# Optimization experiments

Hardware: AMD Instinct MI355X
Metric: run time of the kernel (lower is better)

Reference implementation:

```python
import jax, jax.numpy as jnp
import numpy as np
from jax.ops import segment_sum, segment_max

N_NODES = 10000
N_EDGES = 160000
N_GRAPHS = 32
IN_DIM = 128
HID = 256
HEADS = 4


def setup_inputs() -> dict:
    key = jax.random.key(0)
    ks = jax.random.split(key, 12)
    x = jax.random.normal(ks[0], (N_NODES, IN_DIM), dtype=jnp.float32)
    edge_index = jax.random.randint(ks[1], (2, N_EDGES), 0, N_NODES, dtype=jnp.int64)
    batch = jnp.sort(jax.random.randint(ks[2], (N_NODES,), 0, N_GRAPHS, dtype=jnp.int64))
    s = 0.05
    params = {
        "W1": jax.random.normal(ks[3], (IN_DIM, HID), dtype=jnp.float32) * s,
        "b1": jnp.zeros((HID,), dtype=jnp.float32),
        "W2": jax.random.normal(ks[4], (HID, HID), dtype=jnp.float32) * s,
        "b2": jnp.zeros((HID,), dtype=jnp.float32),
        "Wg": jax.random.normal(ks[5], (HID, HEADS * HID), dtype=jnp.float32) * s,
        "att_src": jax.random.normal(ks[6], (HEADS, HID), dtype=jnp.float32) * s,
        "att_dst": jax.random.normal(ks[7], (HEADS, HID), dtype=jnp.float32) * s,
        "bg": jnp.zeros((HID,), dtype=jnp.float32),
        "W_heads": jax.random.normal(ks[8], (HID, 4), dtype=jnp.float32) * s,
        "b_heads": jnp.zeros((4,), dtype=jnp.float32),
    }
    return {"x": x, "edge_index": edge_index, "batch": batch, **params}


def _add_self_loops(edge_index, n):
    loop = jnp.arange(n, dtype=edge_index.dtype)
    src = jnp.concatenate([edge_index[0], loop])
    dst = jnp.concatenate([edge_index[1], loop])
    return src, dst


def _gcn_conv(x, W, b, src, dst, n):
    # PyG GCNConv: add self-loops, symmetric normalization D^-1/2 A D^-1/2
    h = x @ W                                   # [N, out]
    deg = segment_sum(jnp.ones_like(src, dtype=h.dtype), dst, num_segments=n)
    dinv = jax.lax.rsqrt(jnp.maximum(deg, 1e-12))
    coef = dinv[src] * dinv[dst]                # [E+N]
    out = segment_sum(h[src] * coef[:, None], dst, num_segments=n)
    return out + b


def _gat_conv(x, Wg, att_src, att_dst, bg, src, dst, n):
    # PyG GATConv(heads=4, concat=False): mean over heads, leaky_relu slope 0.2
    h = (x @ Wg).reshape(n, HEADS, HID)         # [N, H, C]
    a_src = jnp.einsum('nhc,hc->nh', h, att_src)
    a_dst = jnp.einsum('nhc,hc->nh', h, att_dst)
    e = jax.nn.leaky_relu(a_src[src] + a_dst[dst], 0.2)   # [E+N, H]
    m = segment_max(e, dst, num_segments=n)
    e = jnp.exp(e - m[dst])
    z = segment_sum(e, dst, num_segments=n)
    alpha = e / (z[dst] + 1e-16)                # softmax over edges into each dst
    out = segment_sum(h[src] * alpha[:, :, None], dst, num_segments=n)  # [N, H, C]
    return out.mean(axis=1) + bg


def reference(x, edge_index, batch, W1, b1, W2, b2, Wg, att_src, att_dst, bg, W_heads, b_heads):
    n = x.shape[0]
    src, dst = _add_self_loops(edge_index, n)
    h1 = jax.nn.relu(_gcn_conv(x, W1, b1, src, dst, n))
    h2 = jax.nn.relu(_gcn_conv(h1, W2, b2, src, dst, n))
    h3 = jax.nn.relu(_gat_conv(h2, Wg, att_src, att_dst, bg, src, dst, n))
    # global_mean_pool
    ones = jnp.ones((n,), dtype=h3.dtype)
    cnt = segment_sum(ones, batch, num_segments=N_GRAPHS)
    pooled = segment_sum(h3, batch, num_segments=N_GRAPHS) / jnp.maximum(cnt, 1.0)[:, None]
    # four scalar heads stacked: cols = [energy_absorption, elastic_modulus, ballistic_limit, penetration_resistance]
    return pooled @ W_heads + b_heads           # [G, 4]
```

## Files before the change

kernel.cpp:

```cpp
#include <hip/hip_runtime.h>
#include <cmath>

#define IN_DIM 128
#define HID 256
#define NHEADS 4
#define NGRAPHS 32

typedef unsigned short u16;
typedef __attribute__((ext_vector_type(8))) short bfrag8;
typedef __attribute__((ext_vector_type(4))) float f32x4;

__device__ __forceinline__ u16 f2bf(float x) {
  unsigned u = __float_as_uint(x);
  unsigned r = (u + 0x7fffu + ((u >> 16) & 1u)) >> 16;
  return (u16)r;
}
__device__ __forceinline__ float bf2f(u16 v) {
  return __uint_as_float(((unsigned)v) << 16);
}
__device__ __forceinline__ float lof(unsigned u) { return __uint_as_float(u << 16); }
__device__ __forceinline__ float hif(unsigned u) { return __uint_as_float(u & 0xffff0000u); }
__device__ __forceinline__ float lrelu02(float x) { return x > 0.f ? x : 0.2f * x; }

__global__ __launch_bounds__(256) void count_edges_k(const int* __restrict__ dst,
                                                     int* __restrict__ cnt, int E) {
  int i = blockIdx.x * 256 + threadIdx.x;
  if (i < E) atomicAdd(&cnt[dst[i]], 1);
}

__global__ __launch_bounds__(1024) void scan_k(const int* __restrict__ cnt,
                                               int* __restrict__ row_ptr,
                                               float* __restrict__ dinv, int n) {
  __shared__ int s_w[16];
  __shared__ int s_tot;
  int tid = threadIdx.x;
  int wv = tid >> 6, lane = tid & 63;
  int carry = 0;
  int nch = (n + 1023) >> 10;
  for (int c = 0; c < nch; c++) {
    int i = (c << 10) + tid;
    int v = (i < n) ? cnt[i] : 0;
    int incl = v;
    #pragma unroll
    for (int off = 1; off < 64; off <<= 1) {
      int t = __shfl_up(incl, off);
      if (lane >= off) incl += t;
    }
    if (lane == 63) s_w[wv] = incl;
    __syncthreads();
    if (tid < 16) {
      int sv = s_w[tid];
      int si = sv;
      #pragma unroll
      for (int off = 1; off < 16; off <<= 1) {
        int t = __shfl_up(si, off, 16);
        if (tid >= off) si += t;
      }
      s_w[tid] = si - sv;
      if (tid == 15) s_tot = si;
    }
    __syncthreads();
    int excl = incl - v + s_w[wv] + carry;
    if (i < n) {
      row_ptr[i] = excl;
      dinv[i] = rsqrtf((float)(v + 1));
    }
    carry += s_tot;
    __syncthreads();
  }
  if (tid == 0) row_ptr[n] = carry;
}

__global__ __launch_bounds__(256) void fill_csr_k(const int* __restrict__ src,
                                                  const int* __restrict__ dst,
                                                  const int* __restrict__ row_ptr,
                                                  int* __restrict__ cursor,
                                                  int* __restrict__ csr_src, int E) {
  int i = blockIdx.x * 256 + threadIdx.x;
  if (i < E) {
    int d = dst[i];
    int p = atomicAdd(&cursor[d], 1);
    csr_src[row_ptr[d] + p] = src[i];
  }
}

__device__ void pack_a_dev(const float* __restrict__ A, u16* __restrict__ Ap,
                           int K, int KT, int wid, int lane) {
  int fm = wid / KT, kt = wid - fm * KT;
  int m = fm * 16 + (lane & 15);
  int kb = kt * 32 + (lane >> 4) * 8;
  const float* src = A + (size_t)m * K + kb;
  float4 v0 = *(const float4*)src;
  float4 v1 = *(const float4*)(src + 4);
  float vv[8] = {v0.x, v0.y, v0.z, v0.w, v1.x, v1.y, v1.z, v1.w};
  u16 hi[8], lo[8];
  #pragma unroll
  for (int j = 0; j < 8; j++) {
    u16 h = f2bf(vv[j]);
    hi[j] = h;
    lo[j] = f2bf(vv[j] - bf2f(h));
  }
  u16* dstp = Ap + ((size_t)fm * KT + kt) * 1024 + lane * 8;
  *(ushort4*)(dstp)       = make_ushort4(hi[0], hi[1], hi[2], hi[3]);
  *(ushort4*)(dstp + 4)   = make_ushort4(hi[4], hi[5], hi[6], hi[7]);
  *(ushort4*)(dstp + 512) = make_ushort4(lo[0], lo[1], lo[2], lo[3]);
  *(ushort4*)(dstp + 516) = make_ushort4(lo[4], lo[5], lo[6], lo[7]);
}

__device__ void pack_b_dev(const float* __restrict__ B, u16* __restrict__ Bp,
                           int N, int KT, int wid, int lane) {
  int fn = wid / KT, kt = wid - fn * KT;
  int n = fn * 16 + (lane & 15);
  int kb = kt * 32 + (lane >> 4) * 8;
  float vv[8];
  #pragma unroll
  for (int j = 0; j < 8; j++) vv[j] = B[(size_t)(kb + j) * N + n];
  u16 hi[8], lo[8];
  #pragma unroll
  for (int j = 0; j < 8; j++) {
    u16 h = f2bf(vv[j]);
    hi[j] = h;
    lo[j] = f2bf(vv[j] - bf2f(h));
  }
  u16* dstp = Bp + ((size_t)fn * KT + kt) * 1024 + lane * 8;
  *(ushort4*)(dstp)       = make_ushort4(hi[0], hi[1], hi[2], hi[3]);
  *(ushort4*)(dstp + 4)   = make_ushort4(hi[4], hi[5], hi[6], hi[7]);
  *(ushort4*)(dstp + 512) = make_ushort4(lo[0], lo[1], lo[2], lo[3]);
  *(ushort4*)(dstp + 516) = make_ushort4(lo[4], lo[5], lo[6], lo[7]);
}

__global__ __launch_bounds__(256) void prep_k(const float* __restrict__ x,
                                              const float* __restrict__ W1,
                                              const float* __restrict__ W2,
                                              const float* __restrict__ Wg,
                                              const float* __restrict__ att_src,
                                              const float* __restrict__ att_dst,
                                              u16* __restrict__ xp,
                                              u16* __restrict__ w1p,
                                              u16* __restrict__ w2p,
                                              u16* __restrict__ wgp,
                                              float* __restrict__ w_s,
                                              float* __restrict__ w_d, int NFM) {
  __shared__ float red_s[4][NHEADS];
  __shared__ float red_d[4][NHEADS];
  int b = blockIdx.x;
  int tid = threadIdx.x;
  int lane = tid & 63;
  int XB = NFM;
  if (b < XB) {
    int wid = b * 4 + (tid >> 6);
    if (wid < NFM * 4) pack_a_dev(x, xp, IN_DIM, 4, wid, lane);
  } else if (b < XB + 16) {
    pack_b_dev(W1, w1p, HID, 4, (b - XB) * 4 + (tid >> 6), lane);
  } else if (b < XB + 48) {
    pack_b_dev(W2, w2p, HID, 8, (b - XB - 16) * 4 + (tid >> 6), lane);
  } else if (b < XB + 176) {
    pack_b_dev(Wg, wgp, NHEADS * HID, 8, (b - XB - 48) * 4 + (tid >> 6), lane);
  } else {
    int k = b - (XB + 176);
    int c = tid, wvv = c >> 6, ln = c & 63;
    #pragma unroll
    for (int h = 0; h < NHEADS; h++) {
      float w = Wg[(size_t)k * (NHEADS * HID) + h * HID + c];
      float vs = w * att_src[h * HID + c];
      float vd = w * att_dst[h * HID + c];
      #pragma unroll
      for (int off = 32; off; off >>= 1) {
        vs += __shfl_xor(vs, off);
        vd += __shfl_xor(vd, off);
      }
      if (ln == 0) { red_s[wvv][h] = vs; red_d[wvv][h] = vd; }
    }
    __syncthreads();
    if (c < NHEADS)
      w_s[k * NHEADS + c] = red_s[0][c] + red_s[1][c] + red_s[2][c] + red_s[3][c];
    else if (c < 2 * NHEADS) {
      int h = c - NHEADS;
      w_d[k * NHEADS + h] = red_d[0][h] + red_d[1][h] + red_d[2][h] + red_d[3][h];
    }
  }
}

template <int KT, int LDC, bool ALO>
__global__ __launch_bounds__(256) void mfma_gemm_k(const u16* __restrict__ Ap,
                                                   const u16* __restrict__ Bp,
                                                   u16* __restrict__ Cb, int M) {
  int tid = threadIdx.x;
  int w = tid >> 6, lane = tid & 63;
  int wm = w >> 1, wn = w & 1;
  int fm0 = blockIdx.y * 4 + wm * 2;
  int fn0 = blockIdx.x * 4 + wn * 2;
  f32x4 acc[2][2] = {};
  #pragma unroll
  for (int kt = 0; kt < KT; kt++) {
    bfrag8 a_hi[2], a_lo[2], b_hi[2], b_lo[2];
    #pragma unroll
    for (int f = 0; f < 2; f++) {
      const u16* pa = Ap + ((size_t)(fm0 + f) * KT + kt) * 1024 + lane * 8;
      a_hi[f] = *(const bfrag8*)pa;
      if constexpr (ALO) a_lo[f] = *(const bfrag8*)(pa + 512);
      const u16* pb = Bp + ((size_t)(fn0 + f) * KT + kt) * 1024 + lane * 8;
      b_hi[f] = *(const bfrag8*)pb;
      b_lo[f] = *(const bfrag8*)(pb + 512);
    }
    #pragma unroll
    for (int f = 0; f < 2; f++) {
      #pragma unroll
      for (int g = 0; g < 2; g++) {
        acc[f][g] = __builtin_amdgcn_mfma_f32_16x16x32_bf16(a_hi[f], b_hi[g], acc[f][g], 0, 0, 0);
        acc[f][g] = __builtin_amdgcn_mfma_f32_16x16x32_bf16(a_hi[f], b_lo[g], acc[f][g], 0, 0, 0);
        if constexpr (ALO)
          acc[f][g] = __builtin_amdgcn_mfma_f32_16x16x32_bf16(a_lo[f], b_hi[g], acc[f][g], 0, 0, 0);
      }
    }
  }
  int r0 = (lane >> 4) * 4;
  int cl = lane & 15;
  #pragma unroll
  for (int f = 0; f < 2; f++) {
    #pragma unroll
    for (int g = 0; g < 2; g++) {
      int col = (fn0 + g) * 16 + cl;
      #pragma unroll
      for (int r = 0; r < 4; r++) {
        int row = (fm0 + f) * 16 + r0 + r;
        if (row < M) Cb[(size_t)row * LDC + col] = f2bf(acc[f][g][r]);
      }
    }
  }
}

template <bool LOGITS, bool PACK_LO>
__global__ __launch_bounds__(256) void gcn_agg_k(const u16* __restrict__ t,
                                                 const int* __restrict__ row_ptr,
                                                 const int* __restrict__ csr_src,
                                                 const float* __restrict__ dinv,
                                                 const float* __restrict__ bias,
                                                 u16* __restrict__ apack,
                                                 const float* __restrict__ w_s,
                                                 const float* __restrict__ w_d,
                                                 float4* __restrict__ a_src4,
                                                 float4* __restrict__ a_dst4, int N) {
  int wv = threadIdx.x >> 6, lane = threadIdx.x & 63;
  int i = blockIdx.x * 4 + wv;
  if (i >= N) return;
  float di = dinv[i];
  int c4 = lane * 4;
  int beg = row_ptr[i], end = row_ptr[i + 1];
  float a0, a1, a2, a3;
  {
    uint2 u = *(const uint2*)&t[(size_t)i * HID + c4];
    float w = di * di;
    a0 = w * lof(u.x); a1 = w * hif(u.x); a2 = w * lof(u.y); a3 = w * hif(u.y);
  }
  int e = beg;
  for (; e + 3 < end; e += 4) {
    int s0 = csr_src[e + 0], s1 = csr_src[e + 1];
    int s2 = csr_src[e + 2], s3 = csr_src[e + 3];
    float w0 = dinv[s0] * di, w1 = dinv[s1] * di;
    float w2 = dinv[s2] * di, w3 = dinv[s3] * di;
    uint2 u0 = *(const uint2*)&t[(size_t)s0 * HID + c4];
    uint2 u1 = *(const uint2*)&t[(size_t)s1 * HID + c4];
    uint2 u2 = *(const uint2*)&t[(size_t)s2 * HID + c4];
    uint2 u3 = *(const uint2*)&t[(size_t)s3 * HID + c4];
    a0 += w0 * lof(u0.x) + w1 * lof(u1.x) + w2 * lof(u2.x) + w3 * lof(u3.x);
    a1 += w0 * hif(u0.x) + w1 * hif(u1.x) + w2 * hif(u2.x) + w3 * hif(u3.x);
    a2 += w0 * lof(u0.y) + w1 * lof(u1.y) + w2 * lof(u2.y) + w3 * lof(u3.y);
    a3 += w0 * hif(u0.y) + w1 * hif(u1.y) + w2 * hif(u2.y) + w3 * hif(u3.y);
  }
  for (; e < end; e++) {
    int s = csr_src[e];
    float w = dinv[s] * di;
    uint2 u = *(const uint2*)&t[(size_t)s * HID + c4];
    a0 += w * lof(u.x); a1 += w * hif(u.x); a2 += w * lof(u.y); a3 += w * hif(u.y);
  }
  float4 bv = *(const float4*)&bias[c4];
  float v0 = fmaxf(a0 + bv.x, 0.f), v1 = fmaxf(a1 + bv.y, 0.f);
  float v2 = fmaxf(a2 + bv.z, 0.f), v3 = fmaxf(a3 + bv.w, 0.f);
  {
    int fm = i >> 4, kt = c4 >> 5;
    int pl = (i & 15) + 16 * ((c4 >> 3) & 3);
    int j0 = c4 & 7;
    size_t base = ((size_t)fm * 8 + kt) * 1024 + pl * 8 + j0;
    u16 h0 = f2bf(v0), h1 = f2bf(v1), h2 = f2bf(v2), h3 = f2bf(v3);
    *(ushort4*)&apack[base] = make_ushort4(h0, h1, h2, h3);
    if constexpr (PACK_LO)
      *(ushort4*)&apack[base + 512] =
          make_ushort4(f2bf(v0 - bf2f(h0)), f2bf(v1 - bf2f(h1)),
                       f2bf(v2 - bf2f(h2)), f2bf(v3 - bf2f(h3)));
  }
  if constexpr (LOGITS) {
    const float4* ws4 = (const float4*)w_s;
    const float4* wd4 = (const float4*)w_d;
    float4 s0 = ws4[c4 + 0], s1 = ws4[c4 + 1], s2 = ws4[c4 + 2], s3 = ws4[c4 + 3];
    float4 d0 = wd4[c4 + 0], d1 = wd4[c4 + 1], d2 = wd4[c4 + 2], d3 = wd4[c4 + 3];
    float ps0 = v0 * s0.x + v1 * s1.x + v2 * s2.x + v3 * s3.x;
    float ps1 = v0 * s0.y + v1 * s1.y + v2 * s2.y + v3 * s3.y;
    float ps2 = v0 * s0.z + v1 * s1.z + v2 * s2.z + v3 * s3.z;
    float ps3 = v0 * s0.w + v1 * s1.w + v2 * s2.w + v3 * s3.w;
    float pd0 = v0 * d0.x + v1 * d1.x + v2 * d2.x + v3 * d3.x;
    float pd1 = v0 * d0.y + v1 * d1.y + v2 * d2.y + v3 * d3.y;
    float pd2 = v0 * d0.z + v1 * d1.z + v2 * d2.z + v3 * d3.z;
    float pd3 = v0 * d0.w + v1 * d1.w + v2 * d2.w + v3 * d3.w;
    #pragma unroll
    for (int off = 32; off; off >>= 1) {
      ps0 += __shfl_xor(ps0, off); ps1 += __shfl_xor(ps1, off);
      ps2 += __shfl_xor(ps2, off); ps3 += __shfl_xor(ps3, off);
      pd0 += __shfl_xor(pd0, off); pd1 += __shfl_xor(pd1, off);
      pd2 += __shfl_xor(pd2, off); pd3 += __shfl_xor(pd3, off);
    }
    if (lane == 0) {
      a_src4[i] = make_float4(ps0, ps1, ps2, ps3);
      a_dst4[i] = make_float4(pd0, pd1, pd2, pd3);
    }
  }
}

#define ACC8(U, AW, O)                                         \
  acc[O + 0] += (AW) * lof((U).x); acc[O + 1] += (AW) * hif((U).x); \
  acc[O + 2] += (AW) * lof((U).y); acc[O + 3] += (AW) * hif((U).y); \
  acc[O + 4] += (AW) * lof((U).z); acc[O + 5] += (AW) * hif((U).z); \
  acc[O + 6] += (AW) * lof((U).w); acc[O + 7] += (AW) * hif((U).w);

__global__ __launch_bounds__(256) void gat_agg_k(const u16* __restrict__ hgT,
                                                 const int* __restrict__ row_ptr,
                                                 const int* __restrict__ csr_src,
                                                 const float4* __restrict__ a_src4,
                                                 const float4* __restrict__ a_dst4,
                                                 const float* __restrict__ bg,
                                                 float* __restrict__ out, int N) {
  __shared__ int s_src[4][64];
  __shared__ float s_al[4][NHEADS][65];
  int wv = threadIdx.x >> 6, lane = threadIdx.x & 63;
  int i = blockIdx.x * 4 + wv;
  if (i >= N) return;
  int beg = row_ptr[i], end = row_ptr[i + 1];
  int deg = end - beg;
  float4 ad = a_dst4[i];
  int hw = lane >> 4;
  float acc[16];
  #pragma unroll
  for (int j = 0; j < 16; j++) acc[j] = 0.f;
  const u16* rowbase = hgT + (size_t)lane * 16;

  int nk;
  if (deg <= 63) {
    int s = (lane < deg) ? csr_src[beg + lane] : i;
    bool valid = (lane <= deg);
    float4 as = a_src4[s];
    float l0 = valid ? lrelu02(as.x + ad.x) : -INFINITY;
    float l1 = valid ? lrelu02(as.y + ad.y) : -INFINITY;
    float l2 = valid ? lrelu02(as.z + ad.z) : -INFINITY;
    float l3 = valid ? lrelu02(as.w + ad.w) : -INFINITY;
    float m0 = l0, m1 = l1, m2 = l2, m3 = l3;
    #pragma unroll
    for (int off = 32; off; off >>= 1) {
      m0 = fmaxf(m0, __shfl_xor(m0, off)); m1 = fmaxf(m1, __shfl_xor(m1, off));
      m2 = fmaxf(m2, __shfl_xor(m2, off)); m3 = fmaxf(m3, __shfl_xor(m3, off));
    }
    float e0 = valid ? expf(l0 - m0) : 0.f;
    float e1 = valid ? expf(l1 - m1) : 0.f;
    float e2 = valid ? expf(l2 - m2) : 0.f;
    float e3 = valid ? expf(l3 - m3) : 0.f;
    float z0 = e0, z1 = e1, z2 = e2, z3 = e3;
    #pragma unroll
    for (int off = 32; off; off >>= 1) {
      z0 += __shfl_xor(z0, off); z1 += __shfl_xor(z1, off);
      z2 += __shfl_xor(z2, off); z3 += __shfl_xor(z3, off);
    }
    s_src[wv][lane] = s;
    s_al[wv][0][lane] = e0 / (z0 + 1e-16f);
    s_al[wv][1][lane] = e1 / (z1 + 1e-16f);
    s_al[wv][2][lane] = e2 / (z2 + 1e-16f);
    s_al[wv][3][lane] = e3 / (z3 + 1e-16f);
    nk = deg + 1;
    int e = 0;
    for (; e + 1 < nk; e += 2) {
      int sa = s_src[wv][e], sb = s_src[wv][e + 1];
      float awa = s_al[wv][hw][e], awb = s_al[wv][hw][e + 1];
      const uint4* ra = (const uint4*)(rowbase + (size_t)sa * 1024);
      const uint4* rb = (const uint4*)(rowbase + (size_t)sb * 1024);
      uint4 ua0 = ra[0], ua1 = ra[1];
      uint4 ub0 = rb[0], ub1 = rb[1];
      ACC8(ua0, awa, 0); ACC8(ua1, awa, 8);
      ACC8(ub0, awb, 0); ACC8(ub1, awb, 8);
    }
    if (e < nk) {
      int sa = s_src[wv][e];
      float awa = s_al[wv][hw][e];
      const uint4* ra = (const uint4*)(rowbase + (size_t)sa * 1024);
      uint4 ua0 = ra[0], ua1 = ra[1];
      ACC8(ua0, awa, 0); ACC8(ua1, awa, 8);
    }
  } else {
    float4 asi = a_src4[i];
    float ls0 = lrelu02(asi.x + ad.x), ls1 = lrelu02(asi.y + ad.y);
    float ls2 = lrelu02(asi.z + ad.z), ls3 = lrelu02(asi.w + ad.w);
    float m0 = ls0, m1 = ls1, m2 = ls2, m3 = ls3;
    for (int e = beg + lane; e < end; e += 64) {
      float4 as = a_src4[csr_src[e]];
      m0 = fmaxf(m0, lrelu02(as.x + ad.x)); m1 = fmaxf(m1, lrelu02(as.y + ad.y));
      m2 = fmaxf(m2, lrelu02(as.z + ad.z)); m3 = fmaxf(m3, lrelu02(as.w + ad.w));
    }
    #pragma unroll
    for (int off = 32; off; off >>= 1) {
      m0 = fmaxf(m0, __shfl_xor(m0, off)); m1 = fmaxf(m1, __shfl_xor(m1, off));
      m2 = fmaxf(m2, __shfl_xor(m2, off)); m3 = fmaxf(m3, __shfl_xor(m3, off));
    }
    float z0 = (lane == 0) ? expf(ls0 - m0) : 0.f;
    float z1 = (lane == 0) ? expf(ls1 - m1) : 0.f;
    float z2 = (lane == 0) ? expf(ls2 - m2) : 0.f;
    float z3 = (lane == 0) ? expf(ls3 - m3) : 0.f;
    for (int e = beg + lane; e < end; e += 64) {
      float4 as = a_src4[csr_src[e]];
      z0 += expf(lrelu02(as.x + ad.x) - m0); z1 += expf(lrelu02(as.y + ad.y) - m1);
      z2 += expf(lrelu02(as.z + ad.z) - m2); z3 += expf(lrelu02(as.w + ad.w) - m3);
    }
    #pragma unroll
    for (int off = 32; off; off >>= 1) {
      z0 += __shfl_xor(z0, off); z1 += __shfl_xor(z1, off);
      z2 += __shfl_xor(z2, off); z3 += __shfl_xor(z3, off);
    }
    float iz0 = 1.f / (z0 + 1e-16f), iz1 = 1.f / (z1 + 1e-16f);
    float iz2 = 1.f / (z2 + 1e-16f), iz3 = 1.f / (z3 + 1e-16f);
    {
      float w0 = expf(ls0 - m0) * iz0, w1 = expf(ls1 - m1) * iz1;
      float w2 = expf(ls2 - m2) * iz2, w3 = expf(ls3 - m3) * iz3;
      float aw = hw == 0 ? w0 : hw == 1 ? w1 : hw == 2 ? w2 : w3;
      const uint4* r = (const uint4*)(rowbase + (size_t)i * 1024);
      uint4 u0 = r[0], u1 = r[1];
      ACC8(u0, aw, 0); ACC8(u1, aw, 8);
    }
    for (int base = beg; base < end; base += 64) {
      int mc = min(64, end - base);
      if (lane < mc) {
        int s = csr_src[base + lane];
        float4 as = a_src4[s];
        s_src[wv][lane] = s;
        s_al[wv][0][lane] = expf(lrelu02(as.x + ad.x) - m0) * iz0;
        s_al[wv][1][lane] = expf(lrelu02(as.y + ad.y) - m1) * iz1;
        s_al[wv][2][lane] = expf(lrelu02(as.z + ad.z) - m2) * iz2;
        s_al[wv][3][lane] = expf(lrelu02(as.w + ad.w) - m3) * iz3;
      }
      for (int e = 0; e < mc; e++) {
        int sa = s_src[wv][e];
        float awa = s_al[wv][hw][e];
        const uint4* ra = (const uint4*)(rowbase + (size_t)sa * 1024);
        uint4 ua0 = ra[0], ua1 = ra[1];
        ACC8(ua0, awa, 0); ACC8(ua1, awa, 8);
      }
    }
  }
  #pragma unroll
  for (int j = 0; j < 16; j++) {
    acc[j] += __shfl_xor(acc[j], 16);
    acc[j] += __shfl_xor(acc[j], 32);
  }
  if (lane < 16) {
    int cb = lane * 16;
    float o[16];
    #pragma unroll
    for (int j = 0; j < 16; j++)
      o[j] = fmaxf(acc[j] * 0.25f + bg[cb + j], 0.f);
    float* op = out + (size_t)i * HID + cb;
    *(float4*)(op + 0)  = make_float4(o[0], o[1], o[2], o[3]);
    *(float4*)(op + 4)  = make_float4(o[4], o[5], o[6], o[7]);
    *(float4*)(op + 8)  = make_float4(o[8], o[9], o[10], o[11]);
    *(float4*)(op + 12) = make_float4(o[12], o[13], o[14], o[15]);
  }
}

#define POOL_CHUNK 50
__global__ __launch_bounds__(256) void pool_acc_k(const float* __restrict__ h3,
                                                  const int* __restrict__ batch,
                                                  float* __restrict__ pooled,
                                                  float* __restrict__ gcnt, int N) {
  int c = threadIdx.x;
  int i0 = blockIdx.x * POOL_CHUNK;
  int i1 = min(i0 + POOL_CHUNK, N);
  if (i0 >= N) return;
  float acc = 0.f;
  int cur = batch[i0];
  int cnt_local = 0;
  for (int i = i0; i < i1; i++) {
    int g = batch[i];
    if (g != cur) {
      atomicAdd(&pooled[cur * HID + c], acc);
      if (c == 0) atomicAdd(&gcnt[cur], (float)cnt_local);
      acc = 0.f;
      cnt_local = 0;
      cur = g;
    }
    acc += h3[(size_t)i * HID + c];
    cnt_local++;
  }
  atomicAdd(&pooled[cur * HID + c], acc);
  if (c == 0) atomicAdd(&gcnt[cur], (float)cnt_local);
}

__global__ __launch_bounds__(128) void head_k(const float* __restrict__ pooled,
                                              const float* __restrict__ gcnt,
                                              const float* __restrict__ W_heads,
                                              const float* __restrict__ b_heads,
                                              float* __restrict__ out) {
  int tid = threadIdx.x;
  if (tid >= NGRAPHS * 4) return;
  int g = tid >> 2, k = tid & 3;
  float invc = 1.f / fmaxf(gcnt[g], 1.f);
  float acc = 0.f;
  for (int c = 0; c < HID; c++) acc += pooled[g * HID + c] * W_heads[c * 4 + k];
  out[g * 4 + k] = acc * invc + b_heads[k];
}

extern "C" void kernel_launch(void* const* d_in, const int* in_sizes, int n_in,
                              void* d_out, int out_size, void* d_ws, size_t ws_size,
                              hipStream_t stream) {
  const float* x = (const float*)d_in[0];
  const int* ei = (const int*)d_in[1];
  const int* batch = (const int*)d_in[2];
  const float* W1 = (const float*)d_in[3];
  const float* b1 = (const float*)d_in[4];
  const float* W2 = (const float*)d_in[5];
  const float* b2 = (const float*)d_in[6];
  const float* Wg = (const float*)d_in[7];
  const float* att_src = (const float*)d_in[8];
  const float* att_dst = (const float*)d_in[9];
  const float* bg = (const float*)d_in[10];
  const float* W_heads = (const float*)d_in[11];
  const float* b_heads = (const float*)d_in[12];
  float* out = (float*)d_out;

  const int N = in_sizes[0] / IN_DIM;
  const int E = in_sizes[1] / 2;
  const int* src = ei;
  const int* dst = ei + E;

  const int NFM = N / 16;
  const int NFMP = ((N + 63) / 64) * 4;

  char* ws = (char*)d_ws;
  size_t off = 0;
  auto take = [&](size_t bytes) -> char* {
    char* p = ws + off;
    off = (off + bytes + 255) & ~(size_t)255;
    return p;
  };
  int* cnt      = (int*)take((size_t)N * 4);
  int* cursor   = (int*)take((size_t)N * 4);
  float* pooled = (float*)take((size_t)NGRAPHS * HID * 4 + NGRAPHS * 4);
  float* gcnt   = pooled + NGRAPHS * HID;
  size_t zero_span = off;
  int* row_ptr  = (int*)take((size_t)(N + 1) * 4);
  int* csr_src  = (int*)take((size_t)E * 4);
  float* dinv   = (float*)take((size_t)N * 4);
  float4* a_src4 = (float4*)take((size_t)N * 16);
  float4* a_dst4 = (float4*)take((size_t)N * 16);
  float* w_s    = (float*)take((size_t)HID * NHEADS * 4);
  float* w_d    = (float*)take((size_t)HID * NHEADS * 4);
  u16*   tb     = (u16*)take((size_t)N * HID * 2);
  float* h3     = (float*)take((size_t)N * HID * 4);
  u16*   hgT    = (u16*)take((size_t)N * NHEADS * HID * 2);
  u16*   xp     = (u16*)take((size_t)NFMP * 4 * 1024 * 2);
  u16*   h1p    = (u16*)take((size_t)NFMP * 8 * 1024 * 2);
  u16*   h2p    = (u16*)take((size_t)NFMP * 8 * 1024 * 2);
  u16*   w1p    = (u16*)take((size_t)16 * 4 * 1024 * 2);
  u16*   w2p    = (u16*)take((size_t)16 * 8 * 1024 * 2);
  u16*   wgp    = (u16*)take((size_t)64 * 8 * 1024 * 2);

  hipMemsetAsync(cnt, 0, zero_span, stream);

  int eb = (E + 255) / 256;
  count_edges_k<<<eb, 256, 0, stream>>>(dst, cnt, E);
  scan_k<<<1, 1024, 0, stream>>>(cnt, row_ptr, dinv, N);
  fill_csr_k<<<eb, 256, 0, stream>>>(src, dst, row_ptr, cursor, csr_src, E);
  prep_k<<<NFM + 176 + 256, 256, 0, stream>>>(x, W1, W2, Wg, att_src, att_dst,
                                              xp, w1p, w2p, wgp, w_s, w_d, NFM);

  int mg64 = (N + 63) / 64;
  int ng4 = (N + 3) / 4;
  mfma_gemm_k<4, HID, true><<<dim3(4, mg64), 256, 0, stream>>>(xp, w1p, tb, N);
  gcn_agg_k<false, true><<<ng4, 256, 0, stream>>>(tb, row_ptr, csr_src, dinv, b1,
                                                  h1p, nullptr, nullptr, nullptr, nullptr, N);
  mfma_gemm_k<8, HID, true><<<dim3(4, mg64), 256, 0, stream>>>(h1p, w2p, tb, N);
  gcn_agg_k<true, false><<<ng4, 256, 0, stream>>>(tb, row_ptr, csr_src, dinv, b2,
                                                  h2p, w_s, w_d, a_src4, a_dst4, N);
  mfma_gemm_k<8, NHEADS * HID, false><<<dim3(16, mg64), 256, 0, stream>>>(h2p, wgp, hgT, N);
  gat_agg_k<<<ng4, 256, 0, stream>>>(hgT, row_ptr, csr_src, a_src4, a_dst4, bg, h3, N);
  int pb = (N + POOL_CHUNK - 1) / POOL_CHUNK;
  pool_acc_k<<<pb, 256, 0, stream>>>(h3, batch, pooled, gcnt, N);
  head_k<<<1, 128, 0, stream>>>(pooled, gcnt, W_heads, b_heads, out);
}
```

Before: 197.2 us.

## Split GCN edges across wave halves and GAT heads across two waves

In the GCN aggregation each half-wave now handles alternating edges with 16-byte loads over 8 channels per lane, and the halves are combined with a cross-half shuffle. The GAT aggregation assigns two waves per node, each covering two heads with one 16-byte load per edge, and merges their partial sums through shared memory after a block barrier. The aim is more memory-level parallelism and less per-lane work for the gather-heavy aggregations. The cost is redundant softmax computation in both waves, an added block-wide sync, and twice as many GAT blocks.

```diff
diff --git a/kernel.cpp b/kernel.cpp
--- a/kernel.cpp
+++ b/kernel.cpp
@@ -21,6 +21,12 @@
 __device__ __forceinline__ float lof(unsigned u) { return __uint_as_float(u << 16); }
 __device__ __forceinline__ float hif(unsigned u) { return __uint_as_float(u & 0xffff0000u); }
 __device__ __forceinline__ float lrelu02(float x) { return x > 0.f ? x : 0.2f * x; }
+
+#define GACC(U, W)                                                   \
+  acc[0] += (W) * lof((U).x); acc[1] += (W) * hif((U).x);            \
+  acc[2] += (W) * lof((U).y); acc[3] += (W) * hif((U).y);            \
+  acc[4] += (W) * lof((U).z); acc[5] += (W) * hif((U).z);            \
+  acc[6] += (W) * lof((U).w); acc[7] += (W) * hif((U).w);
 
 __global__ __launch_bounds__(256) void count_edges_k(const int* __restrict__ dst,
                                                      int* __restrict__ cnt, int E) {
@@ -245,65 +251,76 @@
   int i = blockIdx.x * 4 + wv;
   if (i >= N) return;
   float di = dinv[i];
-  int c4 = lane * 4;
+  int half = lane >> 5;
+  int c8 = (lane & 31) * 8;
   int beg = row_ptr[i], end = row_ptr[i + 1];
-  float a0, a1, a2, a3;
-  {
-    uint2 u = *(const uint2*)&t[(size_t)i * HID + c4];
+  float acc[8];
+  if (half == 0) {
+    uint4 u = *(const uint4*)&t[(size_t)i * HID + c8];
     float w = di * di;
-    a0 = w * lof(u.x); a1 = w * hif(u.x); a2 = w * lof(u.y); a3 = w * hif(u.y);
-  }
-  int e = beg;
-  for (; e + 3 < end; e += 4) {
-    int s0 = csr_src[e + 0], s1 = csr_src[e + 1];
-    int s2 = csr_src[e + 2], s3 = csr_src[e + 3];
+    acc[0] = w * lof(u.x); acc[1] = w * hif(u.x);
+    acc[2] = w * lof(u.y); acc[3] = w * hif(u.y);
+    acc[4] = w * lof(u.z); acc[5] = w * hif(u.z);
+    acc[6] = w * lof(u.w); acc[7] = w * hif(u.w);
+  } else {
+    #pragma unroll
+    for (int j = 0; j < 8; j++) acc[j] = 0.f;
+  }
+  int e = beg + half;
+  for (; e + 2 < end; e += 4) {
+    int s0 = csr_src[e], s1 = csr_src[e + 2];
     float w0 = dinv[s0] * di, w1 = dinv[s1] * di;
-    float w2 = dinv[s2] * di, w3 = dinv[s3] * di;
-    uint2 u0 = *(const uint2*)&t[(size_t)s0 * HID + c4];
-    uint2 u1 = *(const uint2*)&t[(size_t)s1 * HID + c4];
-    uint2 u2 = *(const uint2*)&t[(size_t)s2 * HID + c4];
-    uint2 u3 = *(const uint2*)&t[(size_t)s3 * HID + c4];
-    a0 += w0 * lof(u0.x) + w1 * lof(u1.x) + w2 * lof(u2.x) + w3 * lof(u3.x);
-    a1 += w0 * hif(u0.x) + w1 * hif(u1.x) + w2 * hif(u2.x) + w3 * hif(u3.x);
-    a2 += w0 * lof(u0.y) + w1 * lof(u1.y) + w2 * lof(u2.y) + w3 * lof(u3.y);
-    a3 += w0 * hif(u0.y) + w1 * hif(u1.y) + w2 * hif(u2.y) + w3 * hif(u3.y);
-  }
-  for (; e < end; e++) {
+    uint4 u0 = *(const uint4*)&t[(size_t)s0 * HID + c8];
+    uint4 u1 = *(const uint4*)&t[(size_t)s1 * HID + c8];
+    GACC(u0, w0);
+    GACC(u1, w1);
+  }
+  if (e < end) {
     int s = csr_src[e];
     float w = dinv[s] * di;
-    uint2 u = *(const uint2*)&t[(size_t)s * HID + c4];
-    a0 += w * lof(u.x); a1 += w * hif(u.x); a2 += w * lof(u.y); a3 += w * hif(u.y);
-  }
-  float4 bv = *(const float4*)&bias[c4];
-  float v0 = fmaxf(a0 + bv.x, 0.f), v1 = fmaxf(a1 + bv.y, 0.f);
-  float v2 = fmaxf(a2 + bv.z, 0.f), v3 = fmaxf(a3 + bv.w, 0.f);
-  {
-    int fm = i >> 4, kt = c4 >> 5;
-    int pl = (i & 15) + 16 * ((c4 >> 3) & 3);
-    int j0 = c4 & 7;
-    size_t base = ((size_t)fm * 8 + kt) * 1024 + pl * 8 + j0;
-    u16 h0 = f2bf(v0), h1 = f2bf(v1), h2 = f2bf(v2), h3 = f2bf(v3);
-    *(ushort4*)&apack[base] = make_ushort4(h0, h1, h2, h3);
-    if constexpr (PACK_LO)
+    uint4 u = *(const uint4*)&t[(size_t)s * HID + c8];
+    GACC(u, w);
+  }
+  #pragma unroll
+  for (int j = 0; j < 8; j++) acc[j] += __shfl_xor(acc[j], 32);
+  float4 b0 = *(const float4*)&bias[c8];
+  float4 b1 = *(const float4*)&bias[c8 + 4];
+  float v[8];
+  v[0] = fmaxf(acc[0] + b0.x, 0.f); v[1] = fmaxf(acc[1] + b0.y, 0.f);
+  v[2] = fmaxf(acc[2] + b0.z, 0.f); v[3] = fmaxf(acc[3] + b0.w, 0.f);
+  v[4] = fmaxf(acc[4] + b1.x, 0.f); v[5] = fmaxf(acc[5] + b1.y, 0.f);
+  v[6] = fmaxf(acc[6] + b1.z, 0.f); v[7] = fmaxf(acc[7] + b1.w, 0.f);
+  if (half == 0) {
+    int fm = i >> 4, kt = c8 >> 5;
+    int pl = (i & 15) + 16 * ((c8 >> 3) & 3);
+    size_t base = ((size_t)fm * 8 + kt) * 1024 + pl * 8;
+    u16 h[8];
+    #pragma unroll
+    for (int j = 0; j < 8; j++) h[j] = f2bf(v[j]);
+    *(ushort4*)&apack[base]     = make_ushort4(h[0], h[1], h[2], h[3]);
+    *(ushort4*)&apack[base + 4] = make_ushort4(h[4], h[5], h[6], h[7]);
+    if constexpr (PACK_LO) {
       *(ushort4*)&apack[base + 512] =
-          make_ushort4(f2bf(v0 - bf2f(h0)), f2bf(v1 - bf2f(h1)),
-                       f2bf(v2 - bf2f(h2)), f2bf(v3 - bf2f(h3)));
+          make_ushort4(f2bf(v[0] - bf2f(h[0])), f2bf(v[1] - bf2f(h[1])),
+                       f2bf(v[2] - bf2f(h[2])), f2bf(v[3] - bf2f(h[3])));
+      *(ushort4*)&apack[base + 516] =
+          make_ushort4(f2bf(v[4] - bf2f(h[4])), f2bf(v[5] - bf2f(h[5])),
+                       f2bf(v[6] - bf2f(h[6])), f2bf(v[7] - bf2f(h[7])));
+    }
   }
   if constexpr (LOGITS) {
-    const float4* ws4 = (const float4*)w_s;
-    const float4* wd4 = (const float4*)w_d;
-    float4 s0 = ws4[c4 + 0], s1 = ws4[c4 + 1], s2 = ws4[c4 + 2], s3 = ws4[c4 + 3];
-    float4 d0 = wd4[c4 + 0], d1 = wd4[c4 + 1], d2 = wd4[c4 + 2], d3 = wd4[c4 + 3];
-    float ps0 = v0 * s0.x + v1 * s1.x + v2 * s2.x + v3 * s3.x;
-    float ps1 = v0 * s0.y + v1 * s1.y + v2 * s2.y + v3 * s3.y;
-    float ps2 = v0 * s0.z + v1 * s1.z + v2 * s2.z + v3 * s3.z;
-    float ps3 = v0 * s0.w + v1 * s1.w + v2 * s2.w + v3 * s3.w;
-    float pd0 = v0 * d0.x + v1 * d1.x + v2 * d2.x + v3 * d3.x;
-    float pd1 = v0 * d0.y + v1 * d1.y + v2 * d2.y + v3 * d3.y;
-    float pd2 = v0 * d0.z + v1 * d1.z + v2 * d2.z + v3 * d3.z;
-    float pd3 = v0 * d0.w + v1 * d1.w + v2 * d2.w + v3 * d3.w;
-    #pragma unroll
-    for (int off = 32; off; off >>= 1) {
+    float ps0 = 0.f, ps1 = 0.f, ps2 = 0.f, ps3 = 0.f;
+    float pd0 = 0.f, pd1 = 0.f, pd2 = 0.f, pd3 = 0.f;
+    #pragma unroll
+    for (int j = 0; j < 8; j++) {
+      float4 sv = *(const float4*)&w_s[(c8 + j) * NHEADS];
+      float4 dv = *(const float4*)&w_d[(c8 + j) * NHEADS];
+      float vj = v[j];
+      ps0 += vj * sv.x; ps1 += vj * sv.y; ps2 += vj * sv.z; ps3 += vj * sv.w;
+      pd0 += vj * dv.x; pd1 += vj * dv.y; pd2 += vj * dv.z; pd3 += vj * dv.w;
+    }
+    #pragma unroll
+    for (int off = 16; off; off >>= 1) {
       ps0 += __shfl_xor(ps0, off); ps1 += __shfl_xor(ps1, off);
       ps2 += __shfl_xor(ps2, off); ps3 += __shfl_xor(ps3, off);
       pd0 += __shfl_xor(pd0, off); pd1 += __shfl_xor(pd1, off);
@@ -315,12 +332,6 @@
     }
   }
 }
-
-#define ACC8(U, AW, O)                                         \
-  acc[O + 0] += (AW) * lof((U).x); acc[O + 1] += (AW) * hif((U).x); \
-  acc[O + 2] += (AW) * lof((U).y); acc[O + 3] += (AW) * hif((U).y); \
-  acc[O + 4] += (AW) * lof((U).z); acc[O + 5] += (AW) * hif((U).z); \
-  acc[O + 6] += (AW) * lof((U).w); acc[O + 7] += (AW) * hif((U).w);
 
 __global__ __launch_bounds__(256) void gat_agg_k(const u16* __restrict__ hgT,
                                                  const int* __restrict__ row_ptr,
@@ -330,20 +341,21 @@
                                                  const float* __restrict__ bg,
                                                  float* __restrict__ out, int N) {
   __shared__ int s_src[4][64];
-  __shared__ float s_al[4][NHEADS][65];
+  __shared__ float s_al[4][2][64];
+  __shared__ float s_comb[2][32][9];
   int wv = threadIdx.x >> 6, lane = threadIdx.x & 63;
-  int i = blockIdx.x * 4 + wv;
-  if (i >= N) return;
+  int nodeSlot = wv >> 1, half = wv & 1;
+  int i = blockIdx.x * 2 + nodeSlot;
+  if (i >= N) { __syncthreads(); return; }
   int beg = row_ptr[i], end = row_ptr[i + 1];
   int deg = end - beg;
   float4 ad = a_dst4[i];
-  int hw = lane >> 4;
-  float acc[16];
-  #pragma unroll
-  for (int j = 0; j < 16; j++) acc[j] = 0.f;
-  const u16* rowbase = hgT + (size_t)lane * 16;
-
-  int nk;
+  int hsel = lane >> 5;
+  const u16* rowbase = hgT + half * 512 + lane * 8;
+  float acc[8];
+  #pragma unroll
+  for (int j = 0; j < 8; j++) acc[j] = 0.f;
+
   if (deg <= 63) {
     int s = (lane < deg) ? csr_src[beg + lane] : i;
     bool valid = (lane <= deg);
@@ -369,28 +381,31 @@
       z2 += __shfl_xor(z2, off); z3 += __shfl_xor(z3, off);
     }
     s_src[wv][lane] = s;
-    s_al[wv][0][lane] = e0 / (z0 + 1e-16f);
-    s_al[wv][1][lane] = e1 / (z1 + 1e-16f);
-    s_al[wv][2][lane] = e2 / (z2 + 1e-16f);
-    s_al[wv][3][lane] = e3 / (z3 + 1e-16f);
-    nk = deg + 1;
+    if (half == 0) {
+      s_al[wv][0][lane] = e0 / (z0 + 1e-16f);
+      s_al[wv][1][lane] = e1 / (z1 + 1e-16f);
+    } else {
+      s_al[wv][0][lane] = e2 / (z2 + 1e-16f);
+      s_al[wv][1][lane] = e3 / (z3 + 1e-16f);
+    }
+    int nk = deg + 1;
     int e = 0;
-    for (; e + 1 < nk; e += 2) {
-      int sa = s_src[wv][e], sb = s_src[wv][e + 1];
-      float awa = s_al[wv][hw][e], awb = s_al[wv][hw][e + 1];
-      const uint4* ra = (const uint4*)(rowbase + (size_t)sa * 1024);
-      const uint4* rb = (const uint4*)(rowbase + (size_t)sb * 1024);
-      uint4 ua0 = ra[0], ua1 = ra[1];
-      uint4 ub0 = rb[0], ub1 = rb[1];
-      ACC8(ua0, awa, 0); ACC8(ua1, awa, 8);
-      ACC8(ub0, awb, 0); ACC8(ub1, awb, 8);
-    }
-    if (e < nk) {
+    for (; e + 3 < nk; e += 4) {
+      int sa = s_src[wv][e + 0], sb = s_src[wv][e + 1];
+      int sc = s_src[wv][e + 2], sd = s_src[wv][e + 3];
+      float wa = s_al[wv][hsel][e + 0], wb = s_al[wv][hsel][e + 1];
+      float wc = s_al[wv][hsel][e + 2], wd = s_al[wv][hsel][e + 3];
+      uint4 ua = *(const uint4*)(rowbase + (size_t)sa * 1024);
+      uint4 ub = *(const uint4*)(rowbase + (size_t)sb * 1024);
+      uint4 uc = *(const uint4*)(rowbase + (size_t)sc * 1024);
+      uint4 ud = *(const uint4*)(rowbase + (size_t)sd * 1024);
+      GACC(ua, wa); GACC(ub, wb); GACC(uc, wc); GACC(ud, wd);
+    }
+    for (; e < nk; e++) {
       int sa = s_src[wv][e];
-      float awa = s_al[wv][hw][e];
-      const uint4* ra = (const uint4*)(rowbase + (size_t)sa * 1024);
-      uint4 ua0 = ra[0], ua1 = ra[1];
-      ACC8(ua0, awa, 0); ACC8(ua1, awa, 8);
+      float wa = s_al[wv][hsel][e];
+      uint4 ua = *(const uint4*)(rowbase + (size_t)sa * 1024);
+      GACC(ua, wa);
     }
   } else {
     float4 asi = a_src4[i];
@@ -426,10 +441,9 @@
     {
       float w0 = expf(ls0 - m0) * iz0, w1 = expf(ls1 - m1) * iz1;
       float w2 = expf(ls2 - m2) * iz2, w3 = expf(ls3 - m3) * iz3;
-      float aw = hw == 0 ? w0 : hw == 1 ? w1 : hw == 2 ? w2 : w3;
-      const uint4* r = (const uint4*)(rowbase + (size_t)i * 1024);
-      uint4 u0 = r[0], u1 = r[1];
-      ACC8(u0, aw, 0); ACC8(u1, aw, 8);
+      float aw = (half == 0) ? (hsel == 0 ? w0 : w1) : (hsel == 0 ? w2 : w3);
+      uint4 u = *(const uint4*)(rowbase + (size_t)i * 1024);
+      GACC(u, aw);
     }
     for (int base = beg; base < end; base += 64) {
       int mc = min(64, end - base);
@@ -437,36 +451,38 @@
         int s = csr_src[base + lane];
         float4 as = a_src4[s];
         s_src[wv][lane] = s;
-        s_al[wv][0][lane] = expf(lrelu02(as.x + ad.x) - m0) * iz0;
-        s_al[wv][1][lane] = expf(lrelu02(as.y + ad.y) - m1) * iz1;
-        s_al[wv][2][lane] = expf(lrelu02(as.z + ad.z) - m2) * iz2;
-        s_al[wv][3][lane] = expf(lrelu02(as.w + ad.w) - m3) * iz3;
+        if (half == 0) {
+          s_al[wv][0][lane] = expf(lrelu02(as.x + ad.x) - m0) * iz0;
+          s_al[wv][1][lane] = expf(lrelu02(as.y + ad.y) - m1) * iz1;
+        } else {
+          s_al[wv][0][lane] = expf(lrelu02(as.z + ad.z) - m2) * iz2;
+          s_al[wv][1][lane] = expf(lrelu02(as.w + ad.w) - m3) * iz3;
+        }
       }
       for (int e = 0; e < mc; e++) {
         int sa = s_src[wv][e];
-        float awa = s_al[wv][hw][e];
-        const uint4* ra = (const uint4*)(rowbase + (size_t)sa * 1024);
-        uint4 ua0 = ra[0], ua1 = ra[1];
-        ACC8(ua0, awa, 0); ACC8(ua1, awa, 8);
+        float wa = s_al[wv][hsel][e];
+        uint4 ua = *(const uint4*)(rowbase + (size_t)sa * 1024);
+        GACC(ua, wa);
       }
     }
   }
   #pragma unroll
-  for (int j = 0; j < 16; j++) {
-    acc[j] += __shfl_xor(acc[j], 16);
-    acc[j] += __shfl_xor(acc[j], 32);
-  }
-  if (lane < 16) {
-    int cb = lane * 16;
-    float o[16];
-    #pragma unroll
-    for (int j = 0; j < 16; j++)
-      o[j] = fmaxf(acc[j] * 0.25f + bg[cb + j], 0.f);
+  for (int j = 0; j < 8; j++) acc[j] += __shfl_xor(acc[j], 32);
+  if (half == 1 && lane < 32) {
+    #pragma unroll
+    for (int j = 0; j < 8; j++) s_comb[nodeSlot][lane][j] = acc[j];
+  }
+  __syncthreads();
+  if (half == 0 && lane < 32) {
+    int cb = lane * 8;
+    float o[8];
+    #pragma unroll
+    for (int j = 0; j < 8; j++)
+      o[j] = fmaxf((acc[j] + s_comb[nodeSlot][lane][j]) * 0.25f + bg[cb + j], 0.f);
     float* op = out + (size_t)i * HID + cb;
-    *(float4*)(op + 0)  = make_float4(o[0], o[1], o[2], o[3]);
-    *(float4*)(op + 4)  = make_float4(o[4], o[5], o[6], o[7]);
-    *(float4*)(op + 8)  = make_float4(o[8], o[9], o[10], o[11]);
-    *(float4*)(op + 12) = make_float4(o[12], o[13], o[14], o[15]);
+    *(float4*)(op + 0) = make_float4(o[0], o[1], o[2], o[3]);
+    *(float4*)(op + 4) = make_float4(o[4], o[5], o[6], o[7]);
   }
 }
 
@@ -578,6 +594,7 @@
 
   int mg64 = (N + 63) / 64;
   int ng4 = (N + 3) / 4;
+  int ng2 = (N + 1) / 2;
   mfma_gemm_k<4, HID, true><<<dim3(4, mg64), 256, 0, stream>>>(xp, w1p, tb, N);
   gcn_agg_k<false, true><<<ng4, 256, 0, stream>>>(tb, row_ptr, csr_src, dinv, b1,
                                                   h1p, nullptr, nullptr, nullptr, nullptr, N);
@@ -585,7 +602,7 @@
   gcn_agg_k<true, false><<<ng4, 256, 0, stream>>>(tb, row_ptr, csr_src, dinv, b2,
                                                   h2p, w_s, w_d, a_src4, a_dst4, N);
   mfma_gemm_k<8, NHEADS * HID, false><<<dim3(16, mg64), 256, 0, stream>>>(h2p, wgp, hgT, N);
-  gat_agg_k<<<ng4, 256, 0, stream>>>(hgT, row_ptr, csr_src, a_src4, a_dst4, bg, h3, N);
+  gat_agg_k<<<ng2, 256, 0, stream>>>(hgT, row_ptr, csr_src, a_src4, a_dst4, bg, h3, N);
   int pb = (N + POOL_CHUNK - 1) / POOL_CHUNK;
   pool_acc_k<<<pb, 256, 0, stream>>>(h3, batch, pooled, gcnt, N);
   head_k<<<1, 128, 0, stream>>>(pooled, gcnt, W_heads, b_heads, out);
```

After: 209.0 us. 1.06x slower.
